# Performance work log

Hardware: AMD Instinct MI355X
Metric: run time of the kernel (lower is better)

Reference implementation:

```python
import jax, jax.numpy as jnp
import numpy as np

K = 100  # sliding-window size hard-coded in the original forward


def setup_inputs() -> dict:
    key = jax.random.key(0)
    x = jax.random.normal(key, (32, 1, 1124, 1124), dtype=jnp.float32)
    return {"x": x}


def reference(x):
    # Sliding 100x100 mean over every stride-1 patch (gq == patch mean),
    # computed via a 2D integral image (summed-area table) so we never
    # materialize the [B, C, outH, outW, K, K] patch tensor.
    B, C, H, W = x.shape
    s = jnp.cumsum(jnp.cumsum(x, axis=2), axis=3)
    # pad one zero row/col at the front -> S has shape [B, C, H+1, W+1]
    S = jnp.pad(s, ((0, 0), (0, 0), (1, 0), (1, 0)))
    sums = (S[:, :, K:, K:] - S[:, :, :-K, K:]
            - S[:, :, K:, :-K] + S[:, :, :-K, :-K])  # [B, C, H-K+1, W-K+1]
    # gq averages over the whole patch (all channels + spatial) -> 1 channel out
    out = jnp.sum(sums, axis=1, keepdims=True) / jnp.asarray(K * K * C, x.dtype)
    return out  # [B, 1, H-99, W-99]
```

## Files before the change

kernel.cpp:

```cpp
#include <hip/hip_runtime.h>


#define H_IN    1124
#define W_IN    1124
#define KWIN    100
#define W_OUT   1025
#define H_OUT   1025
#define TSTR    1032
#define NBANDS  24
#define BANDR   43

typedef float    f32x4 __attribute__((ext_vector_type(4)));
typedef _Float16 f16x8 __attribute__((ext_vector_type(8)));

struct alignas(8) h4 { _Float16 a, b, c, d; };

__global__ __launch_bounds__(256) void hslide_kernel(
    const float* __restrict__ x,
    _Float16* __restrict__ T)
{
    __shared__ float srow[W_IN];
    __shared__ float ps[282];

    const int row = blockIdx.x;
    const int tid = threadIdx.x;
    const f32x4* xr4 = (const f32x4*)(x + (size_t)row * W_IN);

    for (int i = tid; i < 281; i += 256)
        ((f32x4*)srow)[i] = __builtin_nontemporal_load(xr4 + i);
    __syncthreads();

    float4 lo = ((const float4*)srow)[tid];
    ps[tid] = lo.x + lo.y + lo.z + lo.w;
    if (tid < 25) {
        float4 v = ((const float4*)srow)[256 + tid];
        ps[256 + tid] = v.x + v.y + v.z + v.w;
    }
    __syncthreads();

    _Float16* trow = T + (size_t)row * TSTR;
    {
        const int w0 = tid * 4;
        float s = 0.f;
        #pragma unroll
        for (int j = 0; j < 25; ++j) s += ps[tid + j];
        float4 hi = ((const float4*)srow)[tid + 25];
        float s1 = s  + hi.x - lo.x;
        float s2 = s1 + hi.y - lo.y;
        float s3 = s2 + hi.z - lo.z;
        *(h4*)(trow + w0) = h4{ (_Float16)s, (_Float16)s1,
                                (_Float16)s2, (_Float16)s3 };
        if (tid == 255) {
            float t = 0.f;
            #pragma unroll
            for (int j = 0; j < 25; ++j) t += ps[256 + j];
            *(h4*)(trow + 1024) = h4{ (_Float16)t, (_Float16)0.f,
                                      (_Float16)0.f, (_Float16)0.f };
            *(h4*)(trow + 1028) = h4{ (_Float16)0.f, (_Float16)0.f,
                                      (_Float16)0.f, (_Float16)0.f };
        }
    }
}

__global__ __launch_bounds__(128) void vslide_kernel(
    const _Float16* __restrict__ T,
    float* __restrict__ out)
{
    const int tid  = threadIdx.x;
    const int band = blockIdx.y;
    const int b    = blockIdx.z;
    const int r0   = band * BANDR;
    const int nr   = min(BANDR, H_OUT - r0);

    const int w0 = tid * 8;
    const _Float16* base  = T + ((size_t)b * H_IN + r0) * TSTR + w0;
    const _Float16* basec = T + ((size_t)b * H_IN + r0) * TSTR + 1024;
    const bool xtra = (tid == 127);
    const float scale = 1.0f / (float)(KWIN * KWIN);

    float s[8];
    #pragma unroll
    for (int j = 0; j < 8; ++j) s[j] = 0.f;
    float s8 = 0.f;

    {
        const _Float16* p  = base;
        const _Float16* pc = basec;
        #pragma unroll 5
        for (int c = 0; c < 25; ++c) {
            f16x8 v0 = *(const f16x8*)(p);
            f16x8 v1 = *(const f16x8*)(p + TSTR);
            f16x8 v2 = *(const f16x8*)(p + 2 * TSTR);
            f16x8 v3 = *(const f16x8*)(p + 3 * TSTR);
            #pragma unroll
            for (int j = 0; j < 8; ++j)
                s[j] += ((float)v0[j] + (float)v1[j])
                      + ((float)v2[j] + (float)v3[j]);
            if (xtra)
                s8 += ((float)pc[0] + (float)pc[TSTR])
                    + ((float)pc[2 * TSTR] + (float)pc[3 * TSTR]);
            p += 4 * TSTR; pc += 4 * TSTR;
        }
    }

    float* q = out + ((size_t)b * H_OUT + r0) * W_OUT + w0;

    #pragma unroll
    for (int j = 0; j < 8; ++j) q[j] = s[j] * scale;
    if (xtra) q[8] = s8 * scale;
    q += W_OUT;

    const _Float16* padd  = base  + (size_t)KWIN * TSTR;
    const _Float16* psub  = base;
    const _Float16* paddc = basec + (size_t)KWIN * TSTR;
    const _Float16* psubc = basec;
    const int steps = nr - 1;
    #pragma unroll 4
    for (int i = 0; i < steps; ++i) {
        f16x8 a = *(const f16x8*)padd;  padd += TSTR;
        f16x8 d = *(const f16x8*)psub;  psub += TSTR;
        #pragma unroll
        for (int j = 0; j < 8; ++j)
            s[j] += (float)a[j] - (float)d[j];
        #pragma unroll
        for (int j = 0; j < 8; ++j) q[j] = s[j] * scale;
        if (xtra) {
            s8 += (float)paddc[0] - (float)psubc[0];
            paddc += TSTR; psubc += TSTR;
            q[8] = s8 * scale;
        }
        q += W_OUT;
    }
}

extern "C" void kernel_launch(void* const* d_in, const int* in_sizes, int n_in,
                              void* d_out, int out_size, void* d_ws, size_t ws_size,
                              hipStream_t stream) {
    const float* x = (const float*)d_in[0];
    float* out     = (float*)d_out;
    _Float16* ws   = (_Float16*)d_ws;

    const int B = 32;
    const size_t perBatchT = (size_t)H_IN * TSTR * sizeof(_Float16);

    int G = (int)(ws_size / perBatchT);
    if (G > B) G = B;
    if (G < 1) G = 1;

    for (int b0 = 0; b0 < B; b0 += G) {
        const int g = (B - b0 < G) ? (B - b0) : G;

        hslide_kernel<<<g * H_IN, 256, 0, stream>>>(
            x + (size_t)b0 * H_IN * W_IN, ws);

        dim3 vgrid(1, NBANDS, g);
        vslide_kernel<<<vgrid, 128, 0, stream>>>(
            ws, out + (size_t)b0 * H_OUT * W_OUT);
    }
}
```

Baseline: 125.0 us.

## Restructure horizontal and vertical sliding-sum kernels with register sliding and column tiling

```diff
diff --git a/kernel.cpp b/kernel.cpp
--- a/kernel.cpp
+++ b/kernel.cpp
@@ -7,58 +7,56 @@
 #define W_OUT   1025
 #define H_OUT   1025
 #define TSTR    1032
-#define NBANDS  24
-#define BANDR   43
+#define NBANDS  16
+#define BANDR   65
 
 typedef float    f32x4 __attribute__((ext_vector_type(4)));
+typedef _Float16 f16x4 __attribute__((ext_vector_type(4)));
 typedef _Float16 f16x8 __attribute__((ext_vector_type(8)));
-
-struct alignas(8) h4 { _Float16 a, b, c, d; };
 
 __global__ __launch_bounds__(256) void hslide_kernel(
     const float* __restrict__ x,
     _Float16* __restrict__ T)
 {
-    __shared__ float srow[W_IN];
-    __shared__ float ps[282];
-
-    const int row = blockIdx.x;
-    const int tid = threadIdx.x;
-    const f32x4* xr4 = (const f32x4*)(x + (size_t)row * W_IN);
-
-    for (int i = tid; i < 281; i += 256)
-        ((f32x4*)srow)[i] = __builtin_nontemporal_load(xr4 + i);
-    __syncthreads();
-
-    float4 lo = ((const float4*)srow)[tid];
-    ps[tid] = lo.x + lo.y + lo.z + lo.w;
-    if (tid < 25) {
-        float4 v = ((const float4*)srow)[256 + tid];
-        ps[256 + tid] = v.x + v.y + v.z + v.w;
-    }
-    __syncthreads();
-
-    _Float16* trow = T + (size_t)row * TSTR;
-    {
-        const int w0 = tid * 4;
-        float s = 0.f;
-        #pragma unroll
-        for (int j = 0; j < 25; ++j) s += ps[tid + j];
-        float4 hi = ((const float4*)srow)[tid + 25];
-        float s1 = s  + hi.x - lo.x;
-        float s2 = s1 + hi.y - lo.y;
-        float s3 = s2 + hi.z - lo.z;
-        *(h4*)(trow + w0) = h4{ (_Float16)s, (_Float16)s1,
-                                (_Float16)s2, (_Float16)s3 };
-        if (tid == 255) {
-            float t = 0.f;
-            #pragma unroll
-            for (int j = 0; j < 25; ++j) t += ps[256 + j];
-            *(h4*)(trow + 1024) = h4{ (_Float16)t, (_Float16)0.f,
-                                      (_Float16)0.f, (_Float16)0.f };
-            *(h4*)(trow + 1028) = h4{ (_Float16)0.f, (_Float16)0.f,
-                                      (_Float16)0.f, (_Float16)0.f };
-        }
+    const int tid   = threadIdx.x;
+    const int chunk = tid & 31;
+    const int lr    = tid >> 5;
+    const int row   = blockIdx.x * 8 + lr;
+    if (row >= H_IN) return;
+    const int b     = blockIdx.y;
+
+    const f32x4* xr = (const f32x4*)(x + ((size_t)b * H_IN + row) * W_IN)
+                    + (size_t)chunk * 8;
+
+    f32x4 lo[8], hi[8];
+    #pragma unroll
+    for (int j = 0; j < 8; ++j) lo[j] = xr[j];
+    #pragma unroll
+    for (int j = 0; j < 8; ++j) hi[j] = xr[25 + j];
+
+    f32x4 acc = lo[0];
+    #pragma unroll
+    for (int j = 1; j < 8; ++j) acc += lo[j];
+    #pragma unroll
+    for (int j = 8; j < 25; ++j) acc += xr[j];
+    float s = (acc.x + acc.y) + (acc.z + acc.w);
+
+    f16x8 pk[4];
+    pk[0][0] = (_Float16)s;
+    #pragma unroll
+    for (int k = 0; k < 31; ++k) {
+        s += hi[k >> 2][k & 3] - lo[k >> 2][k & 3];
+        pk[(k + 1) >> 3][(k + 1) & 7] = (_Float16)s;
+    }
+
+    _Float16* trow = T + ((size_t)b * H_IN + row) * TSTR + chunk * 32;
+    #pragma unroll
+    for (int g2 = 0; g2 < 4; ++g2)
+        *((f16x8*)trow + g2) = pk[g2];
+
+    if (chunk == 31) {
+        float s33 = s + hi[7].w - lo[7].w;
+        trow[32] = (_Float16)s33;
     }
 }
 
@@ -67,69 +65,122 @@
     float* __restrict__ out)
 {
     const int tid  = threadIdx.x;
+    const int tile = blockIdx.x;
     const int band = blockIdx.y;
     const int b    = blockIdx.z;
     const int r0   = band * BANDR;
     const int nr   = min(BANDR, H_OUT - r0);
 
-    const int w0 = tid * 8;
-    const _Float16* base  = T + ((size_t)b * H_IN + r0) * TSTR + w0;
-    const _Float16* basec = T + ((size_t)b * H_IN + r0) * TSTR + 1024;
-    const bool xtra = (tid == 127);
+    const int w0 = tile * 512 + tid * 4;
+    const _Float16* base = T + ((size_t)b * H_IN + r0) * TSTR + w0;
+    const bool xtra = (tile == 1) && (tid == 127);
     const float scale = 1.0f / (float)(KWIN * KWIN);
 
-    float s[8];
-    #pragma unroll
-    for (int j = 0; j < 8; ++j) s[j] = 0.f;
-    float s8 = 0.f;
+    float s0 = 0.f, s1 = 0.f, s2 = 0.f, s3 = 0.f, s8 = 0.f;
 
     {
-        const _Float16* p  = base;
-        const _Float16* pc = basec;
-        #pragma unroll 5
-        for (int c = 0; c < 25; ++c) {
-            f16x8 v0 = *(const f16x8*)(p);
-            f16x8 v1 = *(const f16x8*)(p + TSTR);
-            f16x8 v2 = *(const f16x8*)(p + 2 * TSTR);
-            f16x8 v3 = *(const f16x8*)(p + 3 * TSTR);
+        const _Float16* p = base;
+        #pragma unroll 2
+        for (int cg = 0; cg < 12; ++cg) {
+            f16x4 v[8];
             #pragma unroll
             for (int j = 0; j < 8; ++j)
-                s[j] += ((float)v0[j] + (float)v1[j])
-                      + ((float)v2[j] + (float)v3[j]);
-            if (xtra)
-                s8 += ((float)pc[0] + (float)pc[TSTR])
-                    + ((float)pc[2 * TSTR] + (float)pc[3 * TSTR]);
-            p += 4 * TSTR; pc += 4 * TSTR;
+                v[j] = *(const f16x4*)(p + (size_t)j * TSTR);
+            f16x4 vc[8];
+            if (xtra) {
+                #pragma unroll
+                for (int j = 0; j < 8; ++j)
+                    vc[j] = *(const f16x4*)(p + (size_t)j * TSTR + 4);
+            }
+            #pragma unroll
+            for (int j = 0; j < 8; ++j) {
+                s0 += (float)v[j][0]; s1 += (float)v[j][1];
+                s2 += (float)v[j][2]; s3 += (float)v[j][3];
+            }
+            if (xtra) {
+                #pragma unroll
+                for (int j = 0; j < 8; ++j) s8 += (float)vc[j][0];
+            }
+            p += (size_t)8 * TSTR;
+        }
+        {
+            f16x4 v[4];
+            #pragma unroll
+            for (int j = 0; j < 4; ++j)
+                v[j] = *(const f16x4*)(p + (size_t)j * TSTR);
+            #pragma unroll
+            for (int j = 0; j < 4; ++j) {
+                s0 += (float)v[j][0]; s1 += (float)v[j][1];
+                s2 += (float)v[j][2]; s3 += (float)v[j][3];
+            }
+            if (xtra) {
+                #pragma unroll
+                for (int j = 0; j < 4; ++j)
+                    s8 += (float)*(p + (size_t)j * TSTR + 4);
+            }
         }
     }
 
     float* q = out + ((size_t)b * H_OUT + r0) * W_OUT + w0;
-
-    #pragma unroll
-    for (int j = 0; j < 8; ++j) q[j] = s[j] * scale;
-    if (xtra) q[8] = s8 * scale;
+    __builtin_nontemporal_store(s0 * scale, q + 0);
+    __builtin_nontemporal_store(s1 * scale, q + 1);
+    __builtin_nontemporal_store(s2 * scale, q + 2);
+    __builtin_nontemporal_store(s3 * scale, q + 3);
+    if (xtra) __builtin_nontemporal_store(s8 * scale, q + 4);
     q += W_OUT;
 
-    const _Float16* padd  = base  + (size_t)KWIN * TSTR;
-    const _Float16* psub  = base;
-    const _Float16* paddc = basec + (size_t)KWIN * TSTR;
-    const _Float16* psubc = basec;
+    const _Float16* pa = base + (size_t)KWIN * TSTR;
+    const _Float16* pd = base;
     const int steps = nr - 1;
-    #pragma unroll 4
-    for (int i = 0; i < steps; ++i) {
-        f16x8 a = *(const f16x8*)padd;  padd += TSTR;
-        f16x8 d = *(const f16x8*)psub;  psub += TSTR;
+    int i = 0;
+    for (; i + 4 <= steps; i += 4) {
+        f16x4 a[4], d[4], ac[4], dc[4];
         #pragma unroll
-        for (int j = 0; j < 8; ++j)
-            s[j] += (float)a[j] - (float)d[j];
+        for (int j = 0; j < 4; ++j) {
+            a[j] = *(const f16x4*)(pa + (size_t)j * TSTR);
+            d[j] = *(const f16x4*)(pd + (size_t)j * TSTR);
+        }
+        if (xtra) {
+            #pragma unroll
+            for (int j = 0; j < 4; ++j) {
+                ac[j] = *(const f16x4*)(pa + (size_t)j * TSTR + 4);
+                dc[j] = *(const f16x4*)(pd + (size_t)j * TSTR + 4);
+            }
+        }
         #pragma unroll
-        for (int j = 0; j < 8; ++j) q[j] = s[j] * scale;
+        for (int j = 0; j < 4; ++j) {
+            s0 += (float)a[j][0] - (float)d[j][0];
+            s1 += (float)a[j][1] - (float)d[j][1];
+            s2 += (float)a[j][2] - (float)d[j][2];
+            s3 += (float)a[j][3] - (float)d[j][3];
+            __builtin_nontemporal_store(s0 * scale, q + 0);
+            __builtin_nontemporal_store(s1 * scale, q + 1);
+            __builtin_nontemporal_store(s2 * scale, q + 2);
+            __builtin_nontemporal_store(s3 * scale, q + 3);
+            if (xtra) {
+                s8 += (float)ac[j][0] - (float)dc[j][0];
+                __builtin_nontemporal_store(s8 * scale, q + 4);
+            }
+            q += W_OUT;
+        }
+        pa += (size_t)4 * TSTR;
+        pd += (size_t)4 * TSTR;
+    }
+    for (; i < steps; ++i) {
+        f16x4 a = *(const f16x4*)pa, d = *(const f16x4*)pd;
+        s0 += (float)a[0] - (float)d[0];
+        s1 += (float)a[1] - (float)d[1];
+        s2 += (float)a[2] - (float)d[2];
+        s3 += (float)a[3] - (float)d[3];
+        __builtin_nontemporal_store(s0 * scale, q + 0);
+        __builtin_nontemporal_store(s1 * scale, q + 1);
+        __builtin_nontemporal_store(s2 * scale, q + 2);
+        __builtin_nontemporal_store(s3 * scale, q + 3);
         if (xtra) {
-            s8 += (float)paddc[0] - (float)psubc[0];
-            paddc += TSTR; psubc += TSTR;
-            q[8] = s8 * scale;
-        }
-        q += W_OUT;
+            s8 += (float)*(pa + 4) - (float)*(pd + 4);
+            __builtin_nontemporal_store(s8 * scale, q + 4);
+        }
+        pa += TSTR; pd += TSTR; q += W_OUT;
     }
 }
 
@@ -150,10 +201,11 @@
     for (int b0 = 0; b0 < B; b0 += G) {
         const int g = (B - b0 < G) ? (B - b0) : G;
 
-        hslide_kernel<<<g * H_IN, 256, 0, stream>>>(
+        dim3 hgrid((H_IN + 7) / 8, g);
+        hslide_kernel<<<hgrid, 256, 0, stream>>>(
             x + (size_t)b0 * H_IN * W_IN, ws);
 
-        dim3 vgrid(1, NBANDS, g);
+        dim3 vgrid(2, NBANDS, g);
         vslide_kernel<<<vgrid, 128, 0, stream>>>(
             ws, out + (size_t)b0 * H_OUT * W_OUT);
     }
```

New measurement: 183.2 us. +46.5%, slower.

## Remap vertical slide to one column per thread with 2D tiles and nontemporal stores

Applied to the files above, without the earlier changes.

```diff
diff --git a/kernel.cpp b/kernel.cpp
--- a/kernel.cpp
+++ b/kernel.cpp
@@ -7,8 +7,8 @@
 #define W_OUT   1025
 #define H_OUT   1025
 #define TSTR    1032
-#define NBANDS  24
-#define BANDR   43
+#define NBANDS  16
+#define BANDR   65
 
 typedef float    f32x4 __attribute__((ext_vector_type(4)));
 typedef _Float16 f16x8 __attribute__((ext_vector_type(8)));
@@ -62,74 +62,116 @@
     }
 }
 
-__global__ __launch_bounds__(128) void vslide_kernel(
+__global__ __launch_bounds__(256) void vslide_kernel(
     const _Float16* __restrict__ T,
     float* __restrict__ out)
 {
     const int tid  = threadIdx.x;
+    const int tile = blockIdx.x;
     const int band = blockIdx.y;
     const int b    = blockIdx.z;
     const int r0   = band * BANDR;
     const int nr   = min(BANDR, H_OUT - r0);
-
-    const int w0 = tid * 8;
-    const _Float16* base  = T + ((size_t)b * H_IN + r0) * TSTR + w0;
-    const _Float16* basec = T + ((size_t)b * H_IN + r0) * TSTR + 1024;
-    const bool xtra = (tid == 127);
+    if (nr <= 0) return;
+
+    const int c0 = tile * 512;
+    const bool xtra = (tile == 1) && (tid == 0);
     const float scale = 1.0f / (float)(KWIN * KWIN);
 
-    float s[8];
-    #pragma unroll
-    for (int j = 0; j < 8; ++j) s[j] = 0.f;
-    float s8 = 0.f;
+    const _Float16* baseA = T + ((size_t)b * H_IN + r0) * TSTR + c0 + tid;
+    const _Float16* baseB = baseA + 256;
+    const _Float16* baseC = T + ((size_t)b * H_IN + r0) * TSTR + 1024;
+
+    float sA = 0.f, sB = 0.f, sC = 0.f;
 
     {
-        const _Float16* p  = base;
-        const _Float16* pc = basec;
-        #pragma unroll 5
-        for (int c = 0; c < 25; ++c) {
-            f16x8 v0 = *(const f16x8*)(p);
-            f16x8 v1 = *(const f16x8*)(p + TSTR);
-            f16x8 v2 = *(const f16x8*)(p + 2 * TSTR);
-            f16x8 v3 = *(const f16x8*)(p + 3 * TSTR);
-            #pragma unroll
-            for (int j = 0; j < 8; ++j)
-                s[j] += ((float)v0[j] + (float)v1[j])
-                      + ((float)v2[j] + (float)v3[j]);
-            if (xtra)
-                s8 += ((float)pc[0] + (float)pc[TSTR])
-                    + ((float)pc[2 * TSTR] + (float)pc[3 * TSTR]);
-            p += 4 * TSTR; pc += 4 * TSTR;
-        }
-    }
-
-    float* q = out + ((size_t)b * H_OUT + r0) * W_OUT + w0;
-
-    #pragma unroll
-    for (int j = 0; j < 8; ++j) q[j] = s[j] * scale;
-    if (xtra) q[8] = s8 * scale;
-    q += W_OUT;
-
-    const _Float16* padd  = base  + (size_t)KWIN * TSTR;
-    const _Float16* psub  = base;
-    const _Float16* paddc = basec + (size_t)KWIN * TSTR;
-    const _Float16* psubc = basec;
+        const _Float16* pA = baseA;
+        const _Float16* pB = baseB;
+        const _Float16* pC = baseC;
+        for (int cg = 0; cg < 12; ++cg) {
+            float a[8], c[8];
+            #pragma unroll
+            for (int j = 0; j < 8; ++j) {
+                a[j] = (float)pA[(size_t)j * TSTR];
+                c[j] = (float)pB[(size_t)j * TSTR];
+            }
+            #pragma unroll
+            for (int j = 0; j < 8; ++j) { sA += a[j]; sB += c[j]; }
+            if (xtra) {
+                #pragma unroll
+                for (int j = 0; j < 8; ++j) sC += (float)pC[(size_t)j * TSTR];
+            }
+            pA += (size_t)8 * TSTR; pB += (size_t)8 * TSTR; pC += (size_t)8 * TSTR;
+        }
+        #pragma unroll
+        for (int j = 0; j < 4; ++j) {
+            sA += (float)pA[(size_t)j * TSTR];
+            sB += (float)pB[(size_t)j * TSTR];
+            if (xtra) sC += (float)pC[(size_t)j * TSTR];
+        }
+    }
+
+    float* qrow = out + ((size_t)b * H_OUT + r0) * W_OUT;
+    __builtin_nontemporal_store(sA * scale, qrow + c0 + tid);
+    __builtin_nontemporal_store(sB * scale, qrow + c0 + tid + 256);
+    if (xtra) __builtin_nontemporal_store(sC * scale, qrow + 1024);
+    qrow += W_OUT;
+
+    const _Float16* aA = baseA + (size_t)KWIN * TSTR;
+    const _Float16* aB = baseB + (size_t)KWIN * TSTR;
+    const _Float16* aC = baseC + (size_t)KWIN * TSTR;
+    const _Float16* dA = baseA;
+    const _Float16* dB = baseB;
+    const _Float16* dC = baseC;
+
     const int steps = nr - 1;
-    #pragma unroll 4
-    for (int i = 0; i < steps; ++i) {
-        f16x8 a = *(const f16x8*)padd;  padd += TSTR;
-        f16x8 d = *(const f16x8*)psub;  psub += TSTR;
-        #pragma unroll
-        for (int j = 0; j < 8; ++j)
-            s[j] += (float)a[j] - (float)d[j];
-        #pragma unroll
-        for (int j = 0; j < 8; ++j) q[j] = s[j] * scale;
+    int i = 0;
+    for (; i + 8 <= steps; i += 8) {
+        float addA[8], addB[8], subA[8], subB[8];
+        #pragma unroll
+        for (int j = 0; j < 8; ++j) {
+            addA[j] = (float)aA[(size_t)j * TSTR];
+            addB[j] = (float)aB[(size_t)j * TSTR];
+            subA[j] = (float)dA[(size_t)j * TSTR];
+            subB[j] = (float)dB[(size_t)j * TSTR];
+        }
+        float addC[8], subC[8];
         if (xtra) {
-            s8 += (float)paddc[0] - (float)psubc[0];
-            paddc += TSTR; psubc += TSTR;
-            q[8] = s8 * scale;
-        }
-        q += W_OUT;
+            #pragma unroll
+            for (int j = 0; j < 8; ++j) {
+                addC[j] = (float)aC[(size_t)j * TSTR];
+                subC[j] = (float)dC[(size_t)j * TSTR];
+            }
+        }
+        float* q = qrow;
+        #pragma unroll
+        for (int j = 0; j < 8; ++j) {
+            sA += addA[j] - subA[j];
+            sB += addB[j] - subB[j];
+            __builtin_nontemporal_store(sA * scale, q + c0 + tid);
+            __builtin_nontemporal_store(sB * scale, q + c0 + tid + 256);
+            if (xtra) {
+                sC += addC[j] - subC[j];
+                __builtin_nontemporal_store(sC * scale, q + 1024);
+            }
+            q += W_OUT;
+        }
+        qrow = q;
+        aA += (size_t)8 * TSTR; aB += (size_t)8 * TSTR; aC += (size_t)8 * TSTR;
+        dA += (size_t)8 * TSTR; dB += (size_t)8 * TSTR; dC += (size_t)8 * TSTR;
+    }
+    for (; i < steps; ++i) {
+        sA += (float)aA[0] - (float)dA[0];
+        sB += (float)aB[0] - (float)dB[0];
+        __builtin_nontemporal_store(sA * scale, qrow + c0 + tid);
+        __builtin_nontemporal_store(sB * scale, qrow + c0 + tid + 256);
+        if (xtra) {
+            sC += (float)aC[0] - (float)dC[0];
+            __builtin_nontemporal_store(sC * scale, qrow + 1024);
+        }
+        aA += TSTR; aB += TSTR; aC += TSTR;
+        dA += TSTR; dB += TSTR; dC += TSTR;
+        qrow += W_OUT;
     }
 }
 
@@ -153,8 +195,8 @@
         hslide_kernel<<<g * H_IN, 256, 0, stream>>>(
             x + (size_t)b0 * H_IN * W_IN, ws);
 
-        dim3 vgrid(1, NBANDS, g);
-        vslide_kernel<<<vgrid, 128, 0, stream>>>(
+        dim3 vgrid(2, NBANDS, g);
+        vslide_kernel<<<vgrid, 256, 0, stream>>>(
             ws, out + (size_t)b0 * H_OUT * W_OUT);
     }
 }
```

Measured after the change: 135.1 us. +8.1%, slower.
